# Performance work log

Hardware: AMD Instinct MI355X
Metric: run time of the kernel (lower is better)

Reference implementation:

```python
import jax, jax.numpy as jnp
import numpy as np

D = 128          # state_dim
N_RBF = 20       # n radial basis functions
R_CUT = 10.0
N_NODES = 20000
N_EDGES = 320000
N_GRAPHS = 64
N_ATOMS = 10
ROUNDS = 2       # num_message_passing_rounds


def silu(x):
    return x * jax.nn.sigmoid(x)


def setup_inputs() -> dict:
    key = jax.random.key(0)
    ks = jax.random.split(key, 16)

    def p(k, shape, scale=None):
        scale = (1.0 / np.sqrt(shape[0])) if scale is None else scale
        return (jax.random.normal(k, shape, jnp.float32) * scale).astype(jnp.float32)

    return {
        "edge_src": jax.random.randint(ks[0], (N_EDGES,), 0, N_NODES, jnp.int32),
        "edge_dst": jax.random.randint(ks[1], (N_EDGES,), 0, N_NODES, jnp.int32),
        "edge_vec": jax.random.normal(ks[2], (N_EDGES, 3), jnp.float32) * 2.0,
        "atom_types": jax.random.randint(ks[3], (N_NODES,), 0, N_ATOMS, jnp.int32),
        "node_graph_index": jnp.sort(jax.random.randint(ks[4], (N_NODES,), 0, N_GRAPHS, jnp.int32)),
        "embedding": p(ks[5], (N_ATOMS, D), 1.0),
        "phi_w1": p(ks[6], (D, D)), "phi_b1": jnp.zeros((D,), jnp.float32),
        "phi_w2": p(ks[7], (D, 3 * D)), "phi_b2": jnp.zeros((3 * D,), jnp.float32),
        "filt_w": p(ks[8], (N_RBF, 3 * D)), "filt_b": jnp.zeros((3 * D,), jnp.float32),
        "upd_w1": p(ks[9], (2 * D, D)), "upd_b1": jnp.zeros((D,), jnp.float32),
        "upd_w2": p(ks[10], (D, 3 * D)), "upd_b2": jnp.zeros((3 * D,), jnp.float32),
        "U_w": p(ks[11], (D, D)), "V_w": p(ks[12], (D, D)),
        "out_w1": p(ks[13], (D, D)), "out_b1": jnp.zeros((D,), jnp.float32),
        "out_w2": p(ks[14], (D, 1)), "out_b2": jnp.zeros((1,), jnp.float32),
    }


def reference(edge_src, edge_dst, edge_vec, atom_types, node_graph_index,
              embedding, phi_w1, phi_b1, phi_w2, phi_b2, filt_w, filt_b,
              upd_w1, upd_b1, upd_w2, upd_b2, U_w, V_w,
              out_w1, out_b1, out_w2, out_b2):
    # init scalar states from atom-type embedding; vector states zero
    s = embedding[atom_types]                       # [N, D]
    v = jnp.zeros((N_NODES, 3, D), s.dtype)         # [N, 3, D]

    # geometry (constant across rounds)
    r = jnp.linalg.norm(edge_vec, axis=1)           # [E]
    k = jnp.arange(1, N_RBF + 1, dtype=s.dtype)
    rbf = jnp.sin(k[None, :] * jnp.pi * r[:, None] / R_CUT) / r[:, None]   # [E, n]
    fcut = 0.5 * (jnp.cos(jnp.pi * r / R_CUT) + 1.0) * (r < R_CUT)         # [E]
    W = (rbf @ filt_w + filt_b) * fcut[:, None]     # [E, 3D] filter * cosine cutoff
    dirs = edge_vec / r[:, None]                    # [E, 3] unit edge vectors

    for _ in range(ROUNDS):
        # ---- message block ----
        phi = silu(s[edge_src] @ phi_w1 + phi_b1) @ phi_w2 + phi_b2        # [E, 3D]
        m = phi * W
        m1, m2, m3 = m[:, :D], m[:, D:2 * D], m[:, 2 * D:]
        dv = v[edge_src] * m1[:, None, :] + dirs[:, :, None] * m3[:, None, :]  # [E, 3, D]
        s = s + jax.ops.segment_sum(m2, edge_dst, num_segments=N_NODES)
        v = v + jax.ops.segment_sum(dv, edge_dst, num_segments=N_NODES)

        # ---- update block ----
        U = v @ U_w                                  # [N, 3, D]
        Vp = v @ V_w                                 # [N, 3, D]
        UV = jnp.sum(U * Vp, axis=1)                 # [N, D]
        Vn = jnp.linalg.norm(Vp, axis=1)             # [N, D]
        a = silu(jnp.concatenate([Vn, s], axis=1) @ upd_w1 + upd_b1) @ upd_w2 + upd_b2  # [N, 3D]
        avv, asv, ass = a[:, :D], a[:, D:2 * D], a[:, 2 * D:]
        s = s + ass + UV * asv
        v = v + U * avv[:, None, :]

    # graph readout: index_add over node_graph_index, then output MLP
    g = jax.ops.segment_sum(s, node_graph_index, num_segments=N_GRAPHS)    # [G, D]
    return (silu(g @ out_w1 + out_b1) @ out_w2 + out_b2).reshape(-1)       # [G]
```

## Files before the change

kernel.cpp:

```cpp
#include <hip/hip_runtime.h>

#define NN 20000
#define NE 320000
#define NG 64
#define D 128
#define D3 384
#define NRBF 20
#define RBF_ROW 24
#define PI_F 3.14159265358979323846f
#define RCUT 10.0f

typedef unsigned int uint;
typedef unsigned short ushort;
typedef __attribute__((ext_vector_type(8))) short bf16x8;
typedef __attribute__((ext_vector_type(4))) float f32x4;
typedef __attribute__((ext_vector_type(2))) float v2f;

__device__ __forceinline__ float silu_f(float x) {
    return x / (1.0f + __expf(-x));
}
__device__ __forceinline__ float b2f(ushort u) {
    return __uint_as_float(((uint)u) << 16);
}
__device__ __forceinline__ ushort f2b(float f) {
    uint u = __float_as_uint(f);
    u = u + 0x7fffu + ((u >> 16) & 1u);
    return (ushort)(u >> 16);
}
__device__ __forceinline__ float plo(uint u) { return __uint_as_float(u << 16); }
__device__ __forceinline__ float phi_(uint u) { return __uint_as_float(u & 0xffff0000u); }

#define MFMA3(acc, aH, aL, bH, bL)                                          \
    acc = __builtin_amdgcn_mfma_f32_16x16x32_bf16(aL, bH, acc, 0, 0, 0);    \
    acc = __builtin_amdgcn_mfma_f32_16x16x32_bf16(aH, bL, acc, 0, 0, 0);    \
    acc = __builtin_amdgcn_mfma_f32_16x16x32_bf16(aH, bH, acc, 0, 0, 0);

__global__ __launch_bounds__(256) void mega_init(
    float* __restrict__ g, int* __restrict__ deg,
    const float* __restrict__ pw1, const float* __restrict__ pw2,
    ushort* __restrict__ w1th, ushort* __restrict__ w1tl,
    ushort* __restrict__ w2th, ushort* __restrict__ w2tl,
    const float* __restrict__ Uw, const float* __restrict__ Vw,
    const float* __restrict__ uw1, const float* __restrict__ uw2,
    ushort* __restrict__ uwt, ushort* __restrict__ vwt,
    ushort* __restrict__ u1t, ushort* __restrict__ u2t)
{
    int stride = gridDim.x * blockDim.x;
    int idx0 = blockIdx.x * blockDim.x + threadIdx.x;
    for (int i = idx0; i < NG * D; i += stride) g[i] = 0.f;
    for (int i = idx0; i < NN; i += stride) deg[i] = 0;
    for (int i = idx0; i < D * D; i += stride) {
        int j = i >> 7, k = i & 127;
        float x = pw1[k * D + j]; ushort h = f2b(x);
        w1th[i] = h; w1tl[i] = f2b(x - b2f(h));
        float a = Uw[k * D + j]; ushort ha = f2b(a);
        uwt[i] = ha; uwt[D * D + i] = f2b(a - b2f(ha));
        float b = Vw[k * D + j]; ushort hb = f2b(b);
        vwt[i] = hb; vwt[D * D + i] = f2b(b - b2f(hb));
    }
    for (int i = idx0; i < D3 * D; i += stride) {
        int j = i >> 7, k = i & 127;
        float x = pw2[k * D3 + j]; ushort h = f2b(x);
        w2th[i] = h; w2tl[i] = f2b(x - b2f(h));
        float y = uw2[k * D3 + j]; ushort hy = f2b(y);
        u2t[i] = hy; u2t[D3 * D + i] = f2b(y - b2f(hy));
    }
    for (int i = idx0; i < 2 * D * D; i += stride) {
        int j = i >> 8, k = i & 255;
        float x = uw1[k * D + j]; ushort h = f2b(x);
        u1t[i] = h; u1t[2 * D * D + i] = f2b(x - b2f(h));
    }
}

__global__ __launch_bounds__(1024) void scan_all(
    const int* __restrict__ deg, int* __restrict__ offs,
    int* __restrict__ cursor, int* __restrict__ bpos)
{
    __shared__ int part[1024];
    __shared__ int bc[64];
    int t = threadIdx.x;
    if (t < 64) bc[t] = 0;
    __syncthreads();
    const int per = (NN + 1023) / 1024;
    int base = t * per;
    int sum = 0;
    for (int i = 0; i < per; i++) {
        int idx = base + i;
        if (idx < NN) {
            int dg = deg[idx];
            sum += dg;
            int b = dg > 63 ? 63 : dg;
            atomicAdd(&bc[b], 1);
        }
    }
    part[t] = sum;
    __syncthreads();
    for (int off = 1; off < 1024; off <<= 1) {
        int vv = (t >= off) ? part[t - off] : 0;
        __syncthreads();
        part[t] += vv;
        __syncthreads();
    }
    int run = part[t] - sum;
    for (int i = 0; i < per; i++) {
        int idx = base + i;
        if (idx < NN) {
            offs[idx] = run;
            cursor[idx] = run;
            run += deg[idx];
        }
    }
    if (t == 1023) offs[NN] = run;
    __syncthreads();
    if (t == 0) {
        int r2 = 0;
        for (int b = 63; b >= 0; b--) { bpos[b] = r2; r2 += bc[b]; }
    }
}

__global__ __launch_bounds__(256) void scatter_all(
    const int* __restrict__ dst, int* __restrict__ cursor, int* __restrict__ eid,
    const int* __restrict__ deg, int* __restrict__ bpos, int* __restrict__ perm)
{
    int i = blockIdx.x * blockDim.x + threadIdx.x;
    if (i < NE) {
        int p = atomicAdd(&cursor[dst[i]], 1);
        eid[p] = i;
    }
    if (i < NN) {
        int b = deg[i]; if (b > 63) b = 63;
        int p = atomicAdd(&bpos[b], 1);
        perm[p] = i;
    }
}

__global__ __launch_bounds__(256) void edge_geom_count(
    const float* __restrict__ evec, const int* __restrict__ dst,
    int* __restrict__ deg,
    float* __restrict__ rbf, float4* __restrict__ geo)
{
    int e = blockIdx.x * blockDim.x + threadIdx.x;
    if (e >= NE) return;
    atomicAdd(&deg[dst[e]], 1);
    float x = evec[e * 3 + 0], y = evec[e * 3 + 1], z = evec[e * 3 + 2];
    float r = sqrtf(x * x + y * y + z * z);
    float inv = 1.0f / r;
    float f = (r < RCUT) ? 0.5f * (cosf(PI_F * r / RCUT) + 1.0f) : 0.0f;
    float4 g;
    g.x = x * inv; g.y = y * inv; g.z = z * inv; g.w = f;
    geo[e] = g;
    float base = PI_F * r / RCUT;
    float sf = inv * f;
    #pragma unroll
    for (int k = 0; k < NRBF; k++) {
        rbf[(size_t)e * RBF_ROW + k] = sinf((float)(k + 1) * base) * sf;
    }
}

__global__ __launch_bounds__(128) void phi10(
    const float* __restrict__ emb,
    const float* __restrict__ w1, const float* __restrict__ b1,
    const float* __restrict__ w2, const float* __restrict__ b2,
    uint* __restrict__ ptab)
{
    __shared__ float el[D];
    __shared__ float hl[D];
    int t = blockIdx.x, j = threadIdx.x;
    el[j] = emb[t * D + j];
    __syncthreads();
    float acc = b1[j];
    for (int k = 0; k < D; k++) acc += el[k] * w1[k * D + j];
    hl[j] = silu_f(acc);
    __syncthreads();
    float a1 = b2[D + j], a2 = b2[2 * D + j];
    for (int k = 0; k < D; k++) {
        float h = hl[k];
        a1 += h * w2[k * D3 + D + j];
        a2 += h * w2[k * D3 + 2 * D + j];
    }
    ptab[t * D + j] = (uint)f2b(a1) | ((uint)f2b(a2) << 16);
}

__global__ __launch_bounds__(512)
__attribute__((amdgpu_waves_per_eu(4, 4)))
void node_gather_r0(
    const int* __restrict__ eid, const int* __restrict__ offs,
    const int* __restrict__ perm, const int* __restrict__ src,
    const int* __restrict__ atype, const float* __restrict__ emb,
    const uint* __restrict__ ptab,
    const float* __restrict__ rbf, const float4* __restrict__ geo,
    const float* __restrict__ filt_w, const float* __restrict__ filt_b,
    float* __restrict__ s_new, float* __restrict__ v_new)
{
    int wave = threadIdx.x >> 6;
    int lane = threadIdx.x & 63;
    int widx = blockIdx.x * 4 + (wave >> 1);
    if (widx >= NN) return;
    int node = __builtin_amdgcn_readfirstlane(perm[widx]);
    int half = wave & 1;
    int d = half * 64 + lane;

    v2f wr1v[10], wr2v[10];
    #pragma unroll
    for (int m = 0; m < 10; m++) {
        wr1v[m] = (v2f){filt_w[(2 * m) * D3 + D + d],     filt_w[(2 * m + 1) * D3 + D + d]};
        wr2v[m] = (v2f){filt_w[(2 * m) * D3 + 2 * D + d], filt_w[(2 * m + 1) * D3 + 2 * D + d]};
    }
    float fb1 = filt_b[D + d], fb2 = filt_b[2 * D + d];
    int e0 = __builtin_amdgcn_readfirstlane(offs[node]);
    int e1 = __builtin_amdgcn_readfirstlane(offs[node + 1]);

    float acc_s = 0.f, av0 = 0.f, av1 = 0.f, av2 = 0.f;

    for (int i = e0; i < e1; i += 2) {
        bool hb = (i + 1 < e1);
        int ea = __builtin_amdgcn_readfirstlane(eid[i]);
        int eb = __builtin_amdgcn_readfirstlane(eid[hb ? i + 1 : i]);
        float mb = hb ? 1.0f : 0.0f;
        int sa = __builtin_amdgcn_readfirstlane(src[ea]);
        int sb = __builtin_amdgcn_readfirstlane(src[eb]);
        int ta = __builtin_amdgcn_readfirstlane(atype[sa]);
        int tb = __builtin_amdgcn_readfirstlane(atype[sb]);
        float4 ga = geo[ea];
        float4 gb = geo[eb];
        const float* rpa = rbf + (size_t)ea * RBF_ROW;
        const float* rpb = rbf + (size_t)eb * RBF_ROW;
        uint pka = ptab[ta * D + d];
        uint pkb = ptab[tb * D + d];

        v2f Wa1v = {0.f, 0.f}, Wa2v = {0.f, 0.f};
        v2f Wb1v = {0.f, 0.f}, Wb2v = {0.f, 0.f};
        #pragma unroll
        for (int m = 0; m < 10; m++) {
            float2 ra2 = *(const float2*)(rpa + 2 * m);
            float2 rb2 = *(const float2*)(rpb + 2 * m);
            v2f rav = {ra2.x, ra2.y};
            v2f rbv = {rb2.x, rb2.y};
            Wa1v += rav * wr1v[m]; Wa2v += rav * wr2v[m];
            Wb1v += rbv * wr1v[m]; Wb2v += rbv * wr2v[m];
        }
        float Wa1 = Wa1v.x + Wa1v.y + ga.w * fb1;
        float Wa2 = Wa2v.x + Wa2v.y + ga.w * fb2;
        float Wb1 = Wb1v.x + Wb1v.y + gb.w * fb1;
        float Wb2 = Wb2v.x + Wb2v.y + gb.w * fb2;

        float pa1 = plo(pka), pa2 = phi_(pka);
        float pb1 = plo(pkb), pb2 = phi_(pkb);

        float m2a = pa1 * Wa1, m3a = pa2 * Wa2;
        float m2b = pb1 * Wb1 * mb, m3b = pb2 * Wb2 * mb;
        acc_s += m2a + m2b;
        av0 += ga.x * m3a + gb.x * m3b;
        av1 += ga.y * m3a + gb.y * m3b;
        av2 += ga.z * m3a + gb.z * m3b;
    }

    int tn = __builtin_amdgcn_readfirstlane(atype[node]);
    s_new[node * D + d] = emb[tn * D + d] + acc_s;
    v_new[(node * 3 + 0) * D + d] = av0;
    v_new[(node * 3 + 1) * D + d] = av1;
    v_new[(node * 3 + 2) * D + d] = av2;
}

__global__ __launch_bounds__(512)
__attribute__((amdgpu_waves_per_eu(4, 4)))
void node_gather(
    const int* __restrict__ eid, const int* __restrict__ offs,
    const int* __restrict__ perm, const int* __restrict__ src,
    const ushort* __restrict__ pv,
    const float* __restrict__ s_old, const float* __restrict__ v_old,
    const float* __restrict__ rbf, const float4* __restrict__ geo,
    const float* __restrict__ filt_w, const float* __restrict__ filt_b,
    float* __restrict__ s_new, float* __restrict__ v_new)
{
    int wave = threadIdx.x >> 6;
    int lane = threadIdx.x & 63;
    int widx = blockIdx.x * 4 + (wave >> 1);
    if (widx >= NN) return;
    int node = __builtin_amdgcn_readfirstlane(perm[widx]);
    int half = wave & 1;
    int d = half * 64 + lane;

    v2f wr0v[10], wr1v[10], wr2v[10];
    #pragma unroll
    for (int m = 0; m < 10; m++) {
        wr0v[m] = (v2f){filt_w[(2 * m) * D3 + d],         filt_w[(2 * m + 1) * D3 + d]};
        wr1v[m] = (v2f){filt_w[(2 * m) * D3 + D + d],     filt_w[(2 * m + 1) * D3 + D + d]};
        wr2v[m] = (v2f){filt_w[(2 * m) * D3 + 2 * D + d], filt_w[(2 * m + 1) * D3 + 2 * D + d]};
    }
    float fb0 = filt_b[d], fb1 = filt_b[D + d], fb2 = filt_b[2 * D + d];
    int e0 = __builtin_amdgcn_readfirstlane(offs[node]);
    int e1 = __builtin_amdgcn_readfirstlane(offs[node + 1]);

    float acc_s = 0.f, av0 = 0.f, av1 = 0.f, av2 = 0.f;
    size_t doff = (size_t)d * 6;

    for (int i = e0; i < e1; i += 2) {
        bool hb = (i + 1 < e1);
        int ea = __builtin_amdgcn_readfirstlane(eid[i]);
        int eb = __builtin_amdgcn_readfirstlane(eid[hb ? i + 1 : i]);
        float mb = hb ? 1.0f : 0.0f;
        int sa = __builtin_amdgcn_readfirstlane(src[ea]);
        int sb = __builtin_amdgcn_readfirstlane(src[eb]);
        float4 ga = geo[ea];
        float4 gb = geo[eb];
        const float* rpa = rbf + (size_t)ea * RBF_ROW;
        const float* rpb = rbf + (size_t)eb * RBF_ROW;
        uint3 pka = *(const uint3*)(pv + (size_t)sa * 768 + doff);
        uint3 pkb = *(const uint3*)(pv + (size_t)sb * 768 + doff);

        v2f Wa0v = {0.f, 0.f}, Wa1v = {0.f, 0.f}, Wa2v = {0.f, 0.f};
        v2f Wb0v = {0.f, 0.f}, Wb1v = {0.f, 0.f}, Wb2v = {0.f, 0.f};
        #pragma unroll
        for (int m = 0; m < 10; m++) {
            float2 ra2 = *(const float2*)(rpa + 2 * m);
            float2 rb2 = *(const float2*)(rpb + 2 * m);
            v2f rav = {ra2.x, ra2.y};
            v2f rbv = {rb2.x, rb2.y};
            Wa0v += rav * wr0v[m]; Wa1v += rav * wr1v[m]; Wa2v += rav * wr2v[m];
            Wb0v += rbv * wr0v[m]; Wb1v += rbv * wr1v[m]; Wb2v += rbv * wr2v[m];
        }
        float Wa0 = Wa0v.x + Wa0v.y + ga.w * fb0;
        float Wa1 = Wa1v.x + Wa1v.y + ga.w * fb1;
        float Wa2 = Wa2v.x + Wa2v.y + ga.w * fb2;
        float Wb0 = Wb0v.x + Wb0v.y + gb.w * fb0;
        float Wb1 = Wb1v.x + Wb1v.y + gb.w * fb1;
        float Wb2 = Wb2v.x + Wb2v.y + gb.w * fb2;

        float pa0 = plo(pka.x), pa1 = phi_(pka.x), pa2 = plo(pka.y);
        float va0 = phi_(pka.y), va1 = plo(pka.z), va2 = phi_(pka.z);
        float pb0 = plo(pkb.x), pb1 = phi_(pkb.x), pb2 = plo(pkb.y);
        float vb0 = phi_(pkb.y), vb1 = plo(pkb.z), vb2 = phi_(pkb.z);

        float m1a = pa0 * Wa0, m2a = pa1 * Wa1, m3a = pa2 * Wa2;
        float m1b = pb0 * Wb0 * mb, m2b = pb1 * Wb1 * mb, m3b = pb2 * Wb2 * mb;
        acc_s += m2a + m2b;
        av0 += va0 * m1a + ga.x * m3a + vb0 * m1b + gb.x * m3b;
        av1 += va1 * m1a + ga.y * m3a + vb1 * m1b + gb.y * m3b;
        av2 += va2 * m1a + ga.z * m3a + vb2 * m1b + gb.z * m3b;
    }

    s_new[node * D + d] = s_old[node * D + d] + acc_s;
    v_new[(node * 3 + 0) * D + d] = v_old[(node * 3 + 0) * D + d] + av0;
    v_new[(node * 3 + 1) * D + d] = v_old[(node * 3 + 1) * D + d] + av1;
    v_new[(node * 3 + 2) * D + d] = v_old[(node * 3 + 2) * D + d] + av2;
}

template<bool FUSE>
__global__ __launch_bounds__(256) void node_vupd_mfma(
    float* __restrict__ s, float* __restrict__ v, ushort* __restrict__ pv,
    const int* __restrict__ gi, float* __restrict__ g,
    const ushort* __restrict__ uwt, const ushort* __restrict__ vwt,
    const ushort* __restrict__ u1t, const ushort* __restrict__ u2t,
    const float* __restrict__ ub1, const float* __restrict__ ub2,
    const ushort* __restrict__ w1th, const ushort* __restrict__ w1tl,
    const float* __restrict__ pb1,
    const ushort* __restrict__ w2th, const ushort* __restrict__ w2tl,
    const float* __restrict__ pb2)
{
    __shared__ __align__(16) char smem[47616];
    ushort* U_lds  = (ushort*)(smem);
    float*  UV_lds = (float*)(smem + 13056);
    ushort* a_hi   = (ushort*)(smem + 21504);
    ushort* a_lo   = a_hi + 48 * 136;
    ushort* x_hi   = (ushort*)(smem + 21504);
    ushort* x_lo   = x_hi + 16 * 264;
    ushort* h_hi   = x_lo + 16 * 264;
    ushort* h_lo   = h_hi + 16 * 136;
    float*  a_out  = (float*)(smem + 21504);

    int tid = threadIdx.x;
    int wave = tid >> 6, lane = tid & 63;
    int arow = lane & 15, kg = lane >> 4;
    int n0 = blockIdx.x * 16;

    #pragma unroll
    for (int it = 0; it < 6; it++) {
        int f4 = it * 256 + tid;
        int row = f4 >> 5;
        int c4 = (f4 & 31) * 4;
        int i = row >> 4, n = row & 15;
        float4 vv = *(const float4*)&v[((size_t)(n0 + n) * 3 + i) * D + c4];
        ushort h0 = f2b(vv.x), h1 = f2b(vv.y), h2 = f2b(vv.z), h3 = f2b(vv.w);
        ushort l0 = f2b(vv.x - b2f(h0)), l1 = f2b(vv.y - b2f(h1));
        ushort l2 = f2b(vv.z - b2f(h2)), l3 = f2b(vv.w - b2f(h3));
        uint2 ph; ph.x = (uint)h0 | ((uint)h1 << 16); ph.y = (uint)h2 | ((uint)h3 << 16);
        uint2 pl; pl.x = (uint)l0 | ((uint)l1 << 16); pl.y = (uint)l2 | ((uint)l3 << 16);
        *(uint2*)&a_hi[row * 136 + c4] = ph;
        *(uint2*)&a_lo[row * 136 + c4] = pl;
    }
    __syncthreads();

    f32x4 accU[3][2], accVp[3][2];
    #pragma unroll
    for (int i = 0; i < 3; i++)
        #pragma unroll
        for (int jtl = 0; jtl < 2; jtl++) {
            accU[i][jtl] = (f32x4){0.f, 0.f, 0.f, 0.f};
            accVp[i][jtl] = (f32x4){0.f, 0.f, 0.f, 0.f};
        }
    #pragma unroll
    for (int i = 0; i < 3; i++) {
        #pragma unroll
        for (int t = 0; t < 4; t++) {
            bf16x8 aH = *(const bf16x8*)&a_hi[(i * 16 + arow) * 136 + t * 32 + kg * 8];
            bf16x8 aL = *(const bf16x8*)&a_lo[(i * 16 + arow) * 136 + t * 32 + kg * 8];
            #pragma unroll
            for (int jtl = 0; jtl < 2; jtl++) {
                int j = (wave * 2 + jtl) * 16 + arow;
                bf16x8 bH = *(const bf16x8*)&uwt[(size_t)j * 128 + t * 32 + kg * 8];
                bf16x8 bL = *(const bf16x8*)&uwt[(size_t)D * D + (size_t)j * 128 + t * 32 + kg * 8];
                MFMA3(accU[i][jtl], aH, aL, bH, bL)
                bf16x8 cH = *(const bf16x8*)&vwt[(size_t)j * 128 + t * 32 + kg * 8];
                bf16x8 cL = *(const bf16x8*)&vwt[(size_t)D * D + (size_t)j * 128 + t * 32 + kg * 8];
                MFMA3(accVp[i][jtl], aH, aL, cH, cL)
            }
        }
    }
    __syncthreads();

    #pragma unroll
    for (int jtl = 0; jtl < 2; jtl++) {
        int jcol = (wave * 2 + jtl) * 16 + arow;
        #pragma unroll
        for (int r = 0; r < 4; r++) {
            int n = kg * 4 + r;
            if (FUSE) {
                #pragma unroll
                for (int i = 0; i < 3; i++)
                    U_lds[(i * 16 + n) * 136 + jcol] = f2b(accU[i][jtl][r]);
            }
            float uv = accU[0][jtl][r] * accVp[0][jtl][r]
                     + accU[1][jtl][r] * accVp[1][jtl][r]
                     + accU[2][jtl][r] * accVp[2][jtl][r];
            float nn = accVp[0][jtl][r] * accVp[0][jtl][r]
                     + accVp[1][jtl][r] * accVp[1][jtl][r]
                     + accVp[2][jtl][r] * accVp[2][jtl][r];
            UV_lds[n * 132 + jcol] = uv;
            float vn = sqrtf(nn);
            ushort hh = f2b(vn);
            x_hi[n * 264 + jcol] = hh;
            x_lo[n * 264 + jcol] = f2b(vn - b2f(hh));
        }
    }
    for (int it = 0; it < 8; it++) {
        int t8 = it * 256 + tid;
        int n = t8 >> 7, j = t8 & 127;
        float sv = s[(size_t)(n0 + n) * D + j];
        ushort hh = f2b(sv);
        x_hi[n * 264 + 128 + j] = hh;
        x_lo[n * 264 + 128 + j] = f2b(sv - b2f(hh));
    }
    __syncthreads();

    {
        f32x4 acc1[2];
        acc1[0] = (f32x4){0.f, 0.f, 0.f, 0.f};
        acc1[1] = (f32x4){0.f, 0.f, 0.f, 0.f};
        #pragma unroll
        for (int t = 0; t < 8; t++) {
            bf16x8 aH = *(const bf16x8*)&x_hi[arow * 264 + t * 32 + kg * 8];
            bf16x8 aL = *(const bf16x8*)&x_lo[arow * 264 + t * 32 + kg * 8];
            #pragma unroll
            for (int jtl = 0; jtl < 2; jtl++) {
                int j = (wave * 2 + jtl) * 16 + arow;
                bf16x8 bH = *(const bf16x8*)&u1t[(size_t)j * 256 + t * 32 + kg * 8];
                bf16x8 bL = *(const bf16x8*)&u1t[(size_t)2 * D * D + (size_t)j * 256 + t * 32 + kg * 8];
                MFMA3(acc1[jtl], aH, aL, bH, bL)
            }
        }
        #pragma unroll
        for (int jtl = 0; jtl < 2; jtl++) {
            int j = (wave * 2 + jtl) * 16 + arow;
            float bias = ub1[j];
            #pragma unroll
            for (int r = 0; r < 4; r++) {
                int n = kg * 4 + r;
                float hv = silu_f(acc1[jtl][r] + bias);
                ushort hh = f2b(hv);
                h_hi[n * 136 + j] = hh;
                h_lo[n * 136 + j] = f2b(hv - b2f(hh));
            }
        }
    }
    __syncthreads();

    f32x4 acc2[6];
    #pragma unroll
    for (int q = 0; q < 6; q++) acc2[q] = (f32x4){0.f, 0.f, 0.f, 0.f};
    #pragma unroll
    for (int t = 0; t < 4; t++) {
        bf16x8 aH = *(const bf16x8*)&h_hi[arow * 136 + t * 32 + kg * 8];
        bf16x8 aL = *(const bf16x8*)&h_lo[arow * 136 + t * 32 + kg * 8];
        #pragma unroll
        for (int q = 0; q < 6; q++) {
            int j = (wave * 6 + q) * 16 + arow;
            bf16x8 bH = *(const bf16x8*)&u2t[(size_t)j * 128 + t * 32 + kg * 8];
            bf16x8 bL = *(const bf16x8*)&u2t[(size_t)D3 * D + (size_t)j * 128 + t * 32 + kg * 8];
            MFMA3(acc2[q], aH, aL, bH, bL)
        }
    }
    __syncthreads();

    #pragma unroll
    for (int q = 0; q < 6; q++) {
        int j = (wave * 6 + q) * 16 + arow;
        float bias = ub2[j];
        #pragma unroll
        for (int r = 0; r < 4; r++)
            a_out[(kg * 4 + r) * 392 + j] = acc2[q][r] + bias;
    }
    __syncthreads();

    float snew_reg[8];
    #pragma unroll
    for (int it = 0; it < 8; it++) {
        int t8 = it * 256 + tid;
        int n = t8 >> 7, j = t8 & 127;
        float a1 = a_out[n * 392 + 128 + j];
        float a2 = a_out[n * 392 + 256 + j];
        size_t sidx = (size_t)(n0 + n) * D + j;
        float snew = s[sidx] + a2 + UV_lds[n * 132 + j] * a1;
        if (FUSE) {
            float a0 = a_out[n * 392 + j];
            s[sidx] = snew;
            snew_reg[it] = snew;
            ushort* pvp = pv + ((size_t)(n0 + n) * 128 + j) * 6;
            #pragma unroll
            for (int i = 0; i < 3; i++) {
                size_t idx = ((size_t)(n0 + n) * 3 + i) * D + j;
                float vf = v[idx] + b2f(U_lds[(i * 16 + n) * 136 + j]) * a0;
                v[idx] = vf;
                pvp[3 + i] = f2b(vf);
            }
        } else {
            int gn = gi[n0 + n];
            atomicAdd(&g[(size_t)gn * D + j], snew);
        }
    }

    if (!FUSE) return;

    __syncthreads();
    #pragma unroll
    for (int it = 0; it < 8; it++) {
        int t8 = it * 256 + tid;
        int n = t8 >> 7, j = t8 & 127;
        float sv = snew_reg[it];
        ushort hh = f2b(sv);
        x_hi[n * 264 + j] = hh;
        x_lo[n * 264 + j] = f2b(sv - b2f(hh));
    }
    __syncthreads();

    {
        f32x4 accp[2];
        accp[0] = (f32x4){0.f, 0.f, 0.f, 0.f};
        accp[1] = (f32x4){0.f, 0.f, 0.f, 0.f};
        #pragma unroll
        for (int t = 0; t < 4; t++) {
            bf16x8 aH = *(const bf16x8*)&x_hi[arow * 264 + t * 32 + kg * 8];
            bf16x8 aL = *(const bf16x8*)&x_lo[arow * 264 + t * 32 + kg * 8];
            #pragma unroll
            for (int jtl = 0; jtl < 2; jtl++) {
                int j = (wave * 2 + jtl) * 16 + arow;
                bf16x8 bH = *(const bf16x8*)&w1th[(size_t)j * 128 + t * 32 + kg * 8];
                bf16x8 bL = *(const bf16x8*)&w1tl[(size_t)j * 128 + t * 32 + kg * 8];
                MFMA3(accp[jtl], aH, aL, bH, bL)
            }
        }
        __syncthreads();
        #pragma unroll
        for (int jtl = 0; jtl < 2; jtl++) {
            int j = (wave * 2 + jtl) * 16 + arow;
            float bias = pb1[j];
            #pragma unroll
            for (int r = 0; r < 4; r++) {
                int n = kg * 4 + r;
                float hv = silu_f(accp[jtl][r] + bias);
                ushort hh = f2b(hv);
                h_hi[n * 136 + j] = hh;
                h_lo[n * 136 + j] = f2b(hv - b2f(hh));
            }
        }
    }
    __syncthreads();

    {
        f32x4 accq[6];
        #pragma unroll
        for (int q = 0; q < 6; q++) accq[q] = (f32x4){0.f, 0.f, 0.f, 0.f};
        #pragma unroll
        for (int t = 0; t < 4; t++) {
            bf16x8 aH = *(const bf16x8*)&h_hi[arow * 136 + t * 32 + kg * 8];
            bf16x8 aL = *(const bf16x8*)&h_lo[arow * 136 + t * 32 + kg * 8];
            #pragma unroll
            for (int q = 0; q < 6; q++) {
                int j = (wave * 6 + q) * 16 + arow;
                bf16x8 bH = *(const bf16x8*)&w2th[(size_t)j * 128 + t * 32 + kg * 8];
                bf16x8 bL = *(const bf16x8*)&w2tl[(size_t)j * 128 + t * 32 + kg * 8];
                MFMA3(accq[q], aH, aL, bH, bL)
            }
        }
        #pragma unroll
        for (int q = 0; q < 6; q++) {
            int j = (wave * 6 + q) * 16 + arow;
            float bias = pb2[j];
            int seg = j >> 7;
            int ch  = j & 127;
            #pragma unroll
            for (int r = 0; r < 4; r++) {
                pv[((size_t)(n0 + kg * 4 + r) * 128 + ch) * 6 + seg] = f2b(accq[q][r] + bias);
            }
        }
    }
}

__global__ __launch_bounds__(128) void out_mlp(
    const float* __restrict__ g,
    const float* __restrict__ w1, const float* __restrict__ b1,
    const float* __restrict__ w2, const float* __restrict__ b2,
    float* __restrict__ out)
{
    __shared__ float gl[D];
    __shared__ float red[2];
    int j = threadIdx.x;
    int gr = blockIdx.x;
    gl[j] = g[gr * D + j];
    __syncthreads();
    float acc = b1[j];
    for (int k = 0; k < D; k++) acc += gl[k] * w1[k * D + j];
    float h = silu_f(acc) * w2[j];
    #pragma unroll
    for (int off = 32; off >= 1; off >>= 1) h += __shfl_down(h, off);
    if ((j & 63) == 0) red[j >> 6] = h;
    __syncthreads();
    if (j == 0) out[gr] = red[0] + red[1] + b2[0];
}

extern "C" void kernel_launch(void* const* d_in, const int* in_sizes, int n_in,
                              void* d_out, int out_size, void* d_ws, size_t ws_size,
                              hipStream_t stream)
{
    const int*   edge_src   = (const int*)  d_in[0];
    const int*   edge_dst   = (const int*)  d_in[1];
    const float* edge_vec   = (const float*)d_in[2];
    const int*   atom_types = (const int*)  d_in[3];
    const int*   node_gi    = (const int*)  d_in[4];
    const float* embedding  = (const float*)d_in[5];
    const float* phi_w1     = (const float*)d_in[6];
    const float* phi_b1     = (const float*)d_in[7];
    const float* phi_w2     = (const float*)d_in[8];
    const float* phi_b2     = (const float*)d_in[9];
    const float* filt_w     = (const float*)d_in[10];
    const float* filt_b     = (const float*)d_in[11];
    const float* upd_w1     = (const float*)d_in[12];
    const float* upd_b1     = (const float*)d_in[13];
    const float* upd_w2     = (const float*)d_in[14];
    const float* upd_b2     = (const float*)d_in[15];
    const float* U_w        = (const float*)d_in[16];
    const float* V_w        = (const float*)d_in[17];
    const float* out_w1     = (const float*)d_in[18];
    const float* out_b1     = (const float*)d_in[19];
    const float* out_w2     = (const float*)d_in[20];
    const float* out_b2     = (const float*)d_in[21];

    float* ws = (float*)d_ws;
    size_t o = 0;
    float* s_a   = ws + o; o += (size_t)NN * D;
    float* s_b   = ws + o; o += (size_t)NN * D;
    float* v_a   = ws + o; o += (size_t)NN * 3 * D;
    float* v_b   = ws + o; o += (size_t)NN * 3 * D;
    float* pv_f  = ws + o; o += (size_t)NN * 384;
    float* rbf_f = ws + o; o += (size_t)NE * RBF_ROW;
    float* geo   = ws + o; o += (size_t)NE * 4;
    float* g     = ws + o; o += (size_t)NG * D;
    float* w1t_f = ws + o; o += (size_t)D * D;
    float* w2t_f = ws + o; o += (size_t)D3 * D;
    float* uwt_f = ws + o; o += (size_t)D * D;
    float* vwt_f = ws + o; o += (size_t)D * D;
    float* u1t_f = ws + o; o += (size_t)2 * D * D;
    float* u2t_f = ws + o; o += (size_t)D3 * D;
    float* ptab_f= ws + o; o += (size_t)10 * D;
    int* deg     = (int*)(ws + o); o += NN;
    int* offs    = (int*)(ws + o); o += NN + 1;
    int* cursor  = (int*)(ws + o); o += NN;
    int* perm    = (int*)(ws + o); o += NN;
    int* bpos    = (int*)(ws + o); o += 64;
    int* eidb    = (int*)(ws + o); o += NE;

    ushort* pv    = (ushort*)pv_f;
    ushort* w1th  = (ushort*)w1t_f;
    ushort* w1tl  = w1th + (size_t)D * D;
    ushort* w2th  = (ushort*)w2t_f;
    ushort* w2tl  = w2th + (size_t)D3 * D;
    ushort* uwt   = (ushort*)uwt_f;
    ushort* vwt   = (ushort*)vwt_f;
    ushort* u1t   = (ushort*)u1t_f;
    ushort* u2t   = (ushort*)u2t_f;
    uint*   ptab  = (uint*)ptab_f;

    mega_init<<<512, 256, 0, stream>>>(g, deg, phi_w1, phi_w2,
                                       w1th, w1tl, w2th, w2tl,
                                       U_w, V_w, upd_w1, upd_w2,
                                       uwt, vwt, u1t, u2t);
    edge_geom_count<<<(NE + 255) / 256, 256, 0, stream>>>(edge_vec, edge_dst, deg,
                                                          rbf_f, (float4*)geo);
    scan_all<<<1, 1024, 0, stream>>>(deg, offs, cursor, bpos);
    scatter_all<<<(NE + 255) / 256, 256, 0, stream>>>(edge_dst, cursor, eidb,
                                                      deg, bpos, perm);
    phi10<<<10, 128, 0, stream>>>(embedding, phi_w1, phi_b1, phi_w2, phi_b2, ptab);

    node_gather_r0<<<NN / 4, 512, 0, stream>>>(eidb, offs, perm, edge_src,
                                               atom_types, embedding, ptab,
                                               rbf_f, (const float4*)geo,
                                               filt_w, filt_b, s_b, v_b);
    node_vupd_mfma<true><<<NN / 16, 256, 0, stream>>>(s_b, v_b, pv, node_gi, g,
                                                      uwt, vwt, u1t, u2t,
                                                      upd_b1, upd_b2,
                                                      w1th, w1tl, phi_b1,
                                                      w2th, w2tl, phi_b2);
    node_gather<<<NN / 4, 512, 0, stream>>>(eidb, offs, perm, edge_src, pv,
                                            s_b, v_b, rbf_f,
                                            (const float4*)geo, filt_w, filt_b,
                                            s_a, v_a);
    node_vupd_mfma<false><<<NN / 16, 256, 0, stream>>>(s_a, v_a, pv, node_gi, g,
                                                       uwt, vwt, u1t, u2t,
                                                       upd_b1, upd_b2,
                                                       w1th, w1tl, phi_b1,
                                                       w2th, w2tl, phi_b2);

    out_mlp<<<NG, 128, 0, stream>>>(g, out_w1, out_b1, out_w2, out_b2, (float*)d_out);
}
```

Measured before the change: 635.1 us.

## Write edge geometry, RBF and source data directly in CSR order

Splits degree counting into its own kernel and merges geometry/RBF computation into the scatter pass, so per-edge geometry, RBF rows, source node ids and source atom types are stored at their CSR position. The gather kernels then read contiguous edge data indexed by CSR slot, which removes the eid->src->atype chain of dependent scalar loads and the random rbf/geo row accesses. The cost is an extra NE-sized source-type array and a scattered write of RBF rows during preprocessing. Atomic ordering within a node's segment is nondeterministic, as it was before.

```diff
diff --git a/kernel.cpp b/kernel.cpp
--- a/kernel.cpp
+++ b/kernel.cpp
@@ -72,6 +72,13 @@
     }
 }
 
+__global__ __launch_bounds__(256) void csr_count(
+    const int* __restrict__ dst, int* __restrict__ deg)
+{
+    int e = blockIdx.x * blockDim.x + threadIdx.x;
+    if (e < NE) atomicAdd(&deg[dst[e]], 1);
+}
+
 __global__ __launch_bounds__(1024) void scan_all(
     const int* __restrict__ deg, int* __restrict__ offs,
     int* __restrict__ cursor, int* __restrict__ bpos)
@@ -118,42 +125,38 @@
     }
 }
 
-__global__ __launch_bounds__(256) void scatter_all(
-    const int* __restrict__ dst, int* __restrict__ cursor, int* __restrict__ eid,
+__global__ __launch_bounds__(256) void geom_scatter(
+    const float* __restrict__ evec, const int* __restrict__ dst,
+    const int* __restrict__ srcv, const int* __restrict__ atype,
+    int* __restrict__ cursor,
+    float* __restrict__ rbf, float4* __restrict__ geo,
+    int* __restrict__ src_csr, int* __restrict__ styp_csr,
     const int* __restrict__ deg, int* __restrict__ bpos, int* __restrict__ perm)
 {
-    int i = blockIdx.x * blockDim.x + threadIdx.x;
-    if (i < NE) {
-        int p = atomicAdd(&cursor[dst[i]], 1);
-        eid[p] = i;
-    }
-    if (i < NN) {
-        int b = deg[i]; if (b > 63) b = 63;
+    int e = blockIdx.x * blockDim.x + threadIdx.x;
+    if (e < NE) {
+        int p = atomicAdd(&cursor[dst[e]], 1);
+        float x = evec[e * 3 + 0], y = evec[e * 3 + 1], z = evec[e * 3 + 2];
+        float r = sqrtf(x * x + y * y + z * z);
+        float inv = 1.0f / r;
+        float f = (r < RCUT) ? 0.5f * (cosf(PI_F * r / RCUT) + 1.0f) : 0.0f;
+        float4 gg;
+        gg.x = x * inv; gg.y = y * inv; gg.z = z * inv; gg.w = f;
+        geo[p] = gg;
+        int sn = srcv[e];
+        src_csr[p] = sn;
+        styp_csr[p] = atype[sn];
+        float base = PI_F * r / RCUT;
+        float sf = inv * f;
+        #pragma unroll
+        for (int k = 0; k < NRBF; k++) {
+            rbf[(size_t)p * RBF_ROW + k] = sinf((float)(k + 1) * base) * sf;
+        }
+    }
+    if (e < NN) {
+        int b = deg[e]; if (b > 63) b = 63;
         int p = atomicAdd(&bpos[b], 1);
-        perm[p] = i;
-    }
-}
-
-__global__ __launch_bounds__(256) void edge_geom_count(
-    const float* __restrict__ evec, const int* __restrict__ dst,
-    int* __restrict__ deg,
-    float* __restrict__ rbf, float4* __restrict__ geo)
-{
-    int e = blockIdx.x * blockDim.x + threadIdx.x;
-    if (e >= NE) return;
-    atomicAdd(&deg[dst[e]], 1);
-    float x = evec[e * 3 + 0], y = evec[e * 3 + 1], z = evec[e * 3 + 2];
-    float r = sqrtf(x * x + y * y + z * z);
-    float inv = 1.0f / r;
-    float f = (r < RCUT) ? 0.5f * (cosf(PI_F * r / RCUT) + 1.0f) : 0.0f;
-    float4 g;
-    g.x = x * inv; g.y = y * inv; g.z = z * inv; g.w = f;
-    geo[e] = g;
-    float base = PI_F * r / RCUT;
-    float sf = inv * f;
-    #pragma unroll
-    for (int k = 0; k < NRBF; k++) {
-        rbf[(size_t)e * RBF_ROW + k] = sinf((float)(k + 1) * base) * sf;
+        perm[p] = e;
     }
 }
 
@@ -184,8 +187,8 @@
 __global__ __launch_bounds__(512)
 __attribute__((amdgpu_waves_per_eu(4, 4)))
 void node_gather_r0(
-    const int* __restrict__ eid, const int* __restrict__ offs,
-    const int* __restrict__ perm, const int* __restrict__ src,
+    const int* __restrict__ offs,
+    const int* __restrict__ perm, const int* __restrict__ styp_csr,
     const int* __restrict__ atype, const float* __restrict__ emb,
     const uint* __restrict__ ptab,
     const float* __restrict__ rbf, const float4* __restrict__ geo,
@@ -214,17 +217,14 @@
 
     for (int i = e0; i < e1; i += 2) {
         bool hb = (i + 1 < e1);
-        int ea = __builtin_amdgcn_readfirstlane(eid[i]);
-        int eb = __builtin_amdgcn_readfirstlane(eid[hb ? i + 1 : i]);
+        int ib = hb ? i + 1 : i;
         float mb = hb ? 1.0f : 0.0f;
-        int sa = __builtin_amdgcn_readfirstlane(src[ea]);
-        int sb = __builtin_amdgcn_readfirstlane(src[eb]);
-        int ta = __builtin_amdgcn_readfirstlane(atype[sa]);
-        int tb = __builtin_amdgcn_readfirstlane(atype[sb]);
-        float4 ga = geo[ea];
-        float4 gb = geo[eb];
-        const float* rpa = rbf + (size_t)ea * RBF_ROW;
-        const float* rpb = rbf + (size_t)eb * RBF_ROW;
+        int ta = __builtin_amdgcn_readfirstlane(styp_csr[i]);
+        int tb = __builtin_amdgcn_readfirstlane(styp_csr[ib]);
+        float4 ga = geo[i];
+        float4 gb = geo[ib];
+        const float* rpa = rbf + (size_t)i * RBF_ROW;
+        const float* rpb = rbf + (size_t)ib * RBF_ROW;
         uint pka = ptab[ta * D + d];
         uint pkb = ptab[tb * D + d];
 
@@ -265,8 +265,8 @@
 __global__ __launch_bounds__(512)
 __attribute__((amdgpu_waves_per_eu(4, 4)))
 void node_gather(
-    const int* __restrict__ eid, const int* __restrict__ offs,
-    const int* __restrict__ perm, const int* __restrict__ src,
+    const int* __restrict__ offs,
+    const int* __restrict__ perm, const int* __restrict__ src_csr,
     const ushort* __restrict__ pv,
     const float* __restrict__ s_old, const float* __restrict__ v_old,
     const float* __restrict__ rbf, const float4* __restrict__ geo,
@@ -297,15 +297,14 @@
 
     for (int i = e0; i < e1; i += 2) {
         bool hb = (i + 1 < e1);
-        int ea = __builtin_amdgcn_readfirstlane(eid[i]);
-        int eb = __builtin_amdgcn_readfirstlane(eid[hb ? i + 1 : i]);
+        int ib = hb ? i + 1 : i;
         float mb = hb ? 1.0f : 0.0f;
-        int sa = __builtin_amdgcn_readfirstlane(src[ea]);
-        int sb = __builtin_amdgcn_readfirstlane(src[eb]);
-        float4 ga = geo[ea];
-        float4 gb = geo[eb];
-        const float* rpa = rbf + (size_t)ea * RBF_ROW;
-        const float* rpb = rbf + (size_t)eb * RBF_ROW;
+        int sa = __builtin_amdgcn_readfirstlane(src_csr[i]);
+        int sb = __builtin_amdgcn_readfirstlane(src_csr[ib]);
+        float4 ga = geo[i];
+        float4 gb = geo[ib];
+        const float* rpa = rbf + (size_t)i * RBF_ROW;
+        const float* rpb = rbf + (size_t)ib * RBF_ROW;
         uint3 pka = *(const uint3*)(pv + (size_t)sa * 768 + doff);
         uint3 pkb = *(const uint3*)(pv + (size_t)sb * 768 + doff);
 
@@ -687,7 +686,8 @@
     int* cursor  = (int*)(ws + o); o += NN;
     int* perm    = (int*)(ws + o); o += NN;
     int* bpos    = (int*)(ws + o); o += 64;
-    int* eidb    = (int*)(ws + o); o += NE;
+    int* src_csr = (int*)(ws + o); o += NE;
+    int* styp_csr= (int*)(ws + o); o += NE;
 
     ushort* pv    = (ushort*)pv_f;
     ushort* w1th  = (ushort*)w1t_f;
@@ -704,14 +704,16 @@
                                        w1th, w1tl, w2th, w2tl,
                                        U_w, V_w, upd_w1, upd_w2,
                                        uwt, vwt, u1t, u2t);
-    edge_geom_count<<<(NE + 255) / 256, 256, 0, stream>>>(edge_vec, edge_dst, deg,
-                                                          rbf_f, (float4*)geo);
+    csr_count<<<(NE + 255) / 256, 256, 0, stream>>>(edge_dst, deg);
     scan_all<<<1, 1024, 0, stream>>>(deg, offs, cursor, bpos);
-    scatter_all<<<(NE + 255) / 256, 256, 0, stream>>>(edge_dst, cursor, eidb,
-                                                      deg, bpos, perm);
+    geom_scatter<<<(NE + 255) / 256, 256, 0, stream>>>(edge_vec, edge_dst, edge_src,
+                                                       atom_types, cursor,
+                                                       rbf_f, (float4*)geo,
+                                                       src_csr, styp_csr,
+                                                       deg, bpos, perm);
     phi10<<<10, 128, 0, stream>>>(embedding, phi_w1, phi_b1, phi_w2, phi_b2, ptab);
 
-    node_gather_r0<<<NN / 4, 512, 0, stream>>>(eidb, offs, perm, edge_src,
+    node_gather_r0<<<NN / 4, 512, 0, stream>>>(offs, perm, styp_csr,
                                                atom_types, embedding, ptab,
                                                rbf_f, (const float4*)geo,
                                                filt_w, filt_b, s_b, v_b);
@@ -720,7 +722,7 @@
                                                       upd_b1, upd_b2,
                                                       w1th, w1tl, phi_b1,
                                                       w2th, w2tl, phi_b2);
-    node_gather<<<NN / 4, 512, 0, stream>>>(eidb, offs, perm, edge_src, pv,
+    node_gather<<<NN / 4, 512, 0, stream>>>(offs, perm, src_csr, pv,
                                             s_b, v_b, rbf_f,
                                             (const float4*)geo, filt_w, filt_b,
                                             s_a, v_a);
```

Result: faster. 603.2 us (-5.0%).
